# Performance work log

Hardware: AMD Instinct MI355X
Metric: run time of the kernel (lower is better)

Reference implementation:

```python
import jax, jax.numpy as jnp
import numpy as np

D_MODEL = 1024
N_HEADS = 16
D_HEAD = 64
D_MLP = 4096
EPS = 1e-5
IGNORE = -1e5
ATTN_SCALE = float(np.sqrt(D_HEAD))


def setup_inputs() -> dict:
    key = jax.random.key(0)
    ks = jax.random.split(key, 10)
    s = 0.02
    return {
        "x": jax.random.normal(ks[0], (2, 2048, D_MODEL), jnp.float32),
        "ln1_w": jnp.ones((D_MODEL,), jnp.float32),
        "ln1_b": jnp.zeros((D_MODEL,), jnp.float32),
        "W_Q": jax.random.normal(ks[1], (N_HEADS, D_MODEL, D_HEAD), jnp.float32) * s,
        "W_K": jax.random.normal(ks[2], (N_HEADS, D_MODEL, D_HEAD), jnp.float32) * s,
        "W_V": jax.random.normal(ks[3], (N_HEADS, D_MODEL, D_HEAD), jnp.float32) * s,
        "W_O": jax.random.normal(ks[4], (N_HEADS, D_HEAD, D_MODEL), jnp.float32) * s,
        "b_Q": jnp.zeros((N_HEADS, D_HEAD), jnp.float32),
        "b_K": jnp.zeros((N_HEADS, D_HEAD), jnp.float32),
        "b_V": jnp.zeros((N_HEADS, D_HEAD), jnp.float32),
        "b_O": jnp.zeros((D_MODEL,), jnp.float32),
        "ln2_w": jnp.ones((D_MODEL,), jnp.float32),
        "ln2_b": jnp.zeros((D_MODEL,), jnp.float32),
        "W_in": jax.random.normal(ks[5], (D_MODEL, D_MLP), jnp.float32) * s,
        "b_in": jnp.zeros((D_MLP,), jnp.float32),
        "W_out": jax.random.normal(ks[6], (D_MLP, D_MODEL), jnp.float32) * s,
        "b_out": jnp.zeros((D_MODEL,), jnp.float32),
    }


def layer_norm(x, w, b):
    x = x - x.mean(axis=-1, keepdims=True)
    scale = jnp.sqrt((x * x).mean(axis=-1, keepdims=True) + EPS)
    return (x / scale) * w + b


def attention(x, W_Q, W_K, W_V, W_O, b_Q, b_K, b_V, b_O):
    # x: [b, s, d_model]; W_{Q,K,V}: [h, d_model, d_head]
    q = jnp.einsum('bsm,hmd->bshd', x, W_Q) + b_Q
    k = jnp.einsum('bsm,hmd->bshd', x, W_K) + b_K
    v = jnp.einsum('bsm,hmd->bshd', x, W_V) + b_V
    scores = jnp.einsum('bqhd,bkhd->bhqk', q, k) / ATTN_SCALE
    s = x.shape[1]
    mask = jnp.tril(jnp.ones((s, s), bool))  # causal
    scores = jnp.where(mask, scores, IGNORE)
    attn = jax.nn.softmax(scores, axis=-1)
    z = jnp.einsum('bkhd,bhqk->bqhd', v, attn)
    return jnp.einsum('bqhd,hdm->bqm', z, W_O) + b_O


def mlp(x, W_in, b_in, W_out, b_out):
    pre = jnp.einsum('bsm,mf->bsf', x, W_in) + b_in
    post = jax.nn.gelu(pre, approximate=False)
    return jnp.einsum('bsf,fm->bsm', post, W_out) + b_out


def reference(x, ln1_w, ln1_b, W_Q, W_K, W_V, W_O, b_Q, b_K, b_V, b_O,
              ln2_w, ln2_b, W_in, b_in, W_out, b_out):
    resid = x + attention(layer_norm(x, ln1_w, ln1_b), W_Q, W_K, W_V, W_O,
                          b_Q, b_K, b_V, b_O)
    out = resid + mlp(layer_norm(resid, ln2_w, ln2_b), W_in, b_in, W_out, b_out)
    return out
```

## Files before the change

### kernel.cpp

```cpp
#include <hip/hip_runtime.h>

typedef __attribute__((ext_vector_type(4))) float f32x4;
typedef __attribute__((ext_vector_type(8))) __bf16 bf16x8;
typedef __attribute__((ext_vector_type(8))) unsigned short ushort8;
typedef __attribute__((ext_vector_type(4))) unsigned short ushort4v;

union UBF8 { ushort8 u; bf16x8 b; };
static __device__ __forceinline__ bf16x8 as_bf(ushort8 v) { UBF8 x; x.u = v; return x.b; }

static __device__ __forceinline__ unsigned short f2bf(float f) {
  union { __bf16 h; unsigned short u; } v; v.h = (__bf16)f; return v.u;
}

static __device__ __forceinline__ unsigned short f2bf_rn(float f) {
  union { float f; unsigned u; } v; v.f = f;
  unsigned r = v.u + 0x7fffu + ((v.u >> 16) & 1u);
  return (unsigned short)(r >> 16);
}

static __device__ __forceinline__ bf16x8 scale8(ushort8 u, float c) {
  ushort8 r;
#pragma unroll
  for (int j = 0; j < 8; j++) {
    union { unsigned u; float f; } t; t.u = ((unsigned)u[j]) << 16;
    r[j] = f2bf_rn(t.f * c);
  }
  return as_bf(r);
}

static __device__ __forceinline__ float gelu_f(float x) {
  return 0.5f * x * (1.0f + erff(x * 0.70710678118654752f));
}

typedef const __attribute__((address_space(1))) void* gas_p;
typedef __attribute__((address_space(3))) void* las_p;
static __device__ __forceinline__ void gload16(const void* g, void* l) {
  __builtin_amdgcn_global_load_lds((gas_p)g, (las_p)l, 16, 0, 0);
}

__global__ __launch_bounds__(256) void ln_kernel(
    const float* __restrict__ in, const float* __restrict__ w,
    const float* __restrict__ b, unsigned short* __restrict__ out)
{
  const int row = blockIdx.x, t = threadIdx.x;
  const float4 v = *reinterpret_cast<const float4*>(in + (size_t)row * 1024 + t * 4);
  float s = v.x + v.y + v.z + v.w;
#pragma unroll
  for (int o = 32; o >= 1; o >>= 1) s += __shfl_xor(s, o);
  __shared__ float ps[4], qs[4];
  if ((t & 63) == 0) ps[t >> 6] = s;
  __syncthreads();
  const float mean = (ps[0] + ps[1] + ps[2] + ps[3]) * (1.0f / 1024.0f);
  const float cx = v.x - mean, cy = v.y - mean, cz = v.z - mean, cw = v.w - mean;
  float q = cx * cx + cy * cy + cz * cz + cw * cw;
#pragma unroll
  for (int o = 32; o >= 1; o >>= 1) q += __shfl_xor(q, o);
  if ((t & 63) == 0) qs[t >> 6] = q;
  __syncthreads();
  const float rstd = rsqrtf((qs[0] + qs[1] + qs[2] + qs[3]) * (1.0f / 1024.0f) + 1e-5f);
  const float4 wv = *reinterpret_cast<const float4*>(w + t * 4);
  const float4 bv = *reinterpret_cast<const float4*>(b + t * 4);
  ushort4v o4;
  o4.x = f2bf(cx * rstd * wv.x + bv.x);
  o4.y = f2bf(cy * rstd * wv.y + bv.y);
  o4.z = f2bf(cz * rstd * wv.z + bv.z);
  o4.w = f2bf(cw * rstd * wv.w + bv.w);
  *reinterpret_cast<ushort4v*>(out + (size_t)row * 1024 + t * 4) = o4;
}

__global__ __launch_bounds__(256) void conv_qkv_kernel(
    const float* __restrict__ WQ, const float* __restrict__ WK,
    const float* __restrict__ WV, unsigned short* __restrict__ out)
{
  __shared__ float t[32][33];
  const int mat_h = blockIdx.z;
  const int mat = mat_h >> 4, h = mat_h & 15;
  const float* W = (mat == 0 ? WQ : (mat == 1 ? WK : WV)) + (size_t)h * (1024 * 64);
  const int m0 = blockIdx.x * 32;
  const int d0 = blockIdx.y * 32;
  const int tx = threadIdx.x & 31, ty = threadIdx.x >> 5;
#pragma unroll
  for (int j = 0; j < 4; j++)
    t[ty + j * 8][tx] = W[(size_t)(m0 + ty + j * 8) * 64 + d0 + tx];
  __syncthreads();
  const size_t obase = (size_t)(mat * 1024 + h * 64 + d0);
#pragma unroll
  for (int j = 0; j < 4; j++)
    out[(obase + ty + j * 8) * 1024 + m0 + tx] = f2bf(t[tx][ty + j * 8]);
}

__global__ __launch_bounds__(256) void pack_bias_kernel(
    const float* __restrict__ bQ, const float* __restrict__ bK,
    const float* __restrict__ bV, float* __restrict__ out)
{
  const int i = blockIdx.x * 256 + threadIdx.x;
  if (i < 1024) out[i] = bQ[i];
  else if (i < 2048) out[i] = bK[i - 1024];
  else if (i < 3072) out[i] = bV[i - 2048];
}

__global__ __launch_bounds__(256) void transpose_cast_kernel(
    const float* __restrict__ in, unsigned short* __restrict__ out, int R, int C)
{
  __shared__ float t[32][33];
  const int c0 = blockIdx.x * 32, r0 = blockIdx.y * 32;
  const int tx = threadIdx.x & 31, ty = threadIdx.x >> 5;
#pragma unroll
  for (int j = 0; j < 4; j++)
    t[ty + j * 8][tx] = in[(size_t)(r0 + ty + j * 8) * C + c0 + tx];
  __syncthreads();
#pragma unroll
  for (int j = 0; j < 4; j++)
    out[(size_t)(c0 + ty + j * 8) * R + r0 + tx] = f2bf(t[tx][ty + j * 8]);
}

template <int BN, int EPI, int WAVES>
__global__ __launch_bounds__(WAVES * 64) void gemm_kernel(
    const unsigned short* __restrict__ A, const unsigned short* __restrict__ Bt,
    void* Cout, const float* __restrict__ bias, const float* resid,
    int N, int K, int gx)
{
  constexpr int BM = 128, BK = 64;
  constexpr int NF = (BN * 2) / (WAVES * 16);
  constexpr int CA = (BM / 8) / WAVES;
  constexpr int CB = (BN / 8) / WAVES;
  __shared__ __align__(16) unsigned short As[2][BM * BK];
  __shared__ __align__(16) unsigned short Bs[2][BN * BK];
  const int tid = threadIdx.x, lane = tid & 63, w = tid >> 6;
  const int nwg = gridDim.x;
  int id = blockIdx.x;
  id = (id & 7) * (nwg >> 3) + (id >> 3);
  const int bm = (id % gx) * BM, bn = (id / gx) * BN;

  const int l15 = lane & 15, hi = lane >> 4;
  const int arow = (WAVES == 8) ? (w >> 2) * 64 : (w >> 1) * 64;
  const int brow = (WAVES == 8) ? (w & 3) * (BN / 4) : (w & 1) * (BN / 2);
  f32x4 acc[4][NF] = {};

  const int srow = lane >> 3;
  const int scol = ((lane & 7) ^ srow) * 8;
  const unsigned short* Ag[CA];
  const unsigned short* Bg[CB];
#pragma unroll
  for (int it = 0; it < CA; it++)
    Ag[it] = A + (size_t)(bm + 8 * (it * WAVES + w) + srow) * K + scol;
#pragma unroll
  for (int it = 0; it < CB; it++)
    Bg[it] = Bt + (size_t)(bn + 8 * (it * WAVES + w) + srow) * K + scol;

  const int rsw = (l15 & 7) << 4;
  const int NT = K / BK;

  auto stage = [&](int k0, int buf) {
#pragma unroll
    for (int it = 0; it < CA; it++)
      gload16(Ag[it] + k0, &As[buf][(it * WAVES + w) * 512]);
#pragma unroll
    for (int it = 0; it < CB; it++)
      gload16(Bg[it] + k0, &Bs[buf][(it * WAVES + w) * 512]);
  };

  stage(0, 0);
  __syncthreads();
  int cur = 0;

  for (int t = 0; t < NT; ++t) {
    if (t + 1 < NT) stage((t + 1) * BK, cur ^ 1);

    const char* Asb = (const char*)As[cur];
    const char* Bsb = (const char*)Bs[cur];
    bf16x8 af[2][4], bfr[2][NF];
#pragma unroll
    for (int kk = 0; kk < 2; kk++) {
      const int cb = kk * 64 + hi * 16;
#pragma unroll
      for (int mf = 0; mf < 4; mf++) {
        const int R = arow + mf * 16 + l15;
        af[kk][mf] = as_bf(*reinterpret_cast<const ushort8*>(Asb + R * (BK * 2) + (cb ^ rsw)));
      }
#pragma unroll
      for (int nf = 0; nf < NF; nf++) {
        const int R = brow + nf * 16 + l15;
        bfr[kk][nf] = as_bf(*reinterpret_cast<const ushort8*>(Bsb + R * (BK * 2) + (cb ^ rsw)));
      }
    }
#pragma unroll
    for (int kk = 0; kk < 2; kk++)
#pragma unroll
      for (int mf = 0; mf < 4; mf++)
#pragma unroll
        for (int nf = 0; nf < NF; nf++)
          acc[mf][nf] = __builtin_amdgcn_mfma_f32_16x16x32_bf16(af[kk][mf], bfr[kk][nf], acc[mf][nf], 0, 0, 0);

    __syncthreads();
    cur ^= 1;
  }

  const int row0 = bm + arow + 4 * hi;
  const int col0 = bn + brow + l15;
#pragma unroll
  for (int mf = 0; mf < 4; mf++) {
#pragma unroll
    for (int nf = 0; nf < NF; nf++) {
#pragma unroll
      for (int i = 0; i < 4; i++) {
        const int row = row0 + mf * 16 + i;
        const int col = col0 + nf * 16;
        float v = acc[mf][nf][i] + bias[col];
        if (EPI == 1) v += resid[(size_t)row * N + col];
        if (EPI == 2) v = gelu_f(v);
        if (EPI == 1) ((float*)Cout)[(size_t)row * N + col] = v;
        else          ((unsigned short*)Cout)[(size_t)row * N + col] = f2bf(v);
      }
    }
  }
}

__global__ __launch_bounds__(256) void attn_kernel(
    const unsigned short* __restrict__ qkv, unsigned short* __restrict__ zout)
{
  __shared__ __align__(16) unsigned short Ks[64 * 72];
  __shared__ __align__(16) unsigned short Vt[64 * 72];
  __shared__ __align__(16) unsigned short Ps[4 * 16 * 72];
  const int tid = threadIdx.x, lane = tid & 63, w = tid >> 6;
  const int l15 = lane & 15, hi = lane >> 4, ko = hi * 8;
  const int j = blockIdx.x, bh = blockIdx.y;
  const int cA = j, cB = 31 - j;
  const size_t tok0 = (size_t)(bh >> 4) * 2048;
  const int h = bh & 15;
  const int qoff = h * 64, koff = 1024 + h * 64, voff = 2048 + h * 64;
  const int rowA = cA * 64 + w * 16;
  const int rowB = cB * 64 + w * 16;
  const float qscale = 0.125f * 1.44269504f;

  bf16x8 qfA[2], qfB[2];
#pragma unroll
  for (int kf = 0; kf < 2; kf++) {
    qfA[kf] = scale8(*reinterpret_cast<const ushort8*>(qkv + (tok0 + rowA + l15) * 3072 + qoff + kf * 32 + ko), qscale);
    qfB[kf] = scale8(*reinterpret_cast<const ushort8*>(qkv + (tok0 + rowB + l15) * 3072 + qoff + kf * 32 + ko), qscale);
  }

  float mA[4], lA[4], mB[4], lB[4];
  f32x4 zA[4], zB[4];
#pragma unroll
  for (int i = 0; i < 4; i++) {
    mA[i] = -1e30f; lA[i] = 0.0f; mB[i] = -1e30f; lB[i] = 0.0f;
#pragma unroll
    for (int nf = 0; nf < 4; nf++) { zA[nf][i] = 0.0f; zB[nf][i] = 0.0f; }
  }

  unsigned short* Pw = Ps + w * (16 * 72);
  const int sr = tid >> 3, scol = (tid & 7) * 8;

  for (int kt = 0; kt <= cB; kt++) {
    __syncthreads();
#pragma unroll
    for (int it = 0; it < 2; it++) {
      const int rr = sr + it * 32;
      const size_t gb = (tok0 + kt * 64 + rr) * 3072;
      *reinterpret_cast<ushort8*>(&Ks[rr * 72 + scol]) =
          *reinterpret_cast<const ushort8*>(qkv + gb + koff + scol);
      ushort8 vv = *reinterpret_cast<const ushort8*>(qkv + gb + voff + scol);
#pragma unroll
      for (int jj = 0; jj < 8; jj++) {
        const int d = scol + jj;
        Vt[d * 72 + (rr ^ (((d >> 3) & 7) << 3))] = vv[jj];
      }
    }
    __syncthreads();

    bf16x8 kb[4][2], vb[4][2];
#pragma unroll
    for (int nf = 0; nf < 4; nf++)
#pragma unroll
      for (int kf = 0; kf < 2; kf++) {
        kb[nf][kf] = as_bf(*reinterpret_cast<const ushort8*>(&Ks[(nf * 16 + l15) * 72 + kf * 32 + ko]));
        const int d = nf * 16 + l15;
        vb[nf][kf] = as_bf(*reinterpret_cast<const ushort8*>(
            &Vt[d * 72 + ((kf * 32 + ko) ^ (((d >> 3) & 7) << 3))]));
      }

    const bool actA = (kt <= cA);

    f32x4 sA[4] = {}, sB[4] = {};
    __builtin_amdgcn_s_setprio(1);
#pragma unroll
    for (int nf = 0; nf < 4; nf++)
#pragma unroll
      for (int kf = 0; kf < 2; kf++) {
        if (actA) sA[nf] = __builtin_amdgcn_mfma_f32_16x16x32_bf16(qfA[kf], kb[nf][kf], sA[nf], 0, 0, 0);
        sB[nf] = __builtin_amdgcn_mfma_f32_16x16x32_bf16(qfB[kf], kb[nf][kf], sB[nf], 0, 0, 0);
      }
    __builtin_amdgcn_s_setprio(0);

    auto process = [&](f32x4* s, float* mrow, float* lrow, f32x4* accz, int rowbase, bool dm) {
#pragma unroll
      for (int i = 0; i < 4; i++) {
        const int rg = rowbase + 4 * hi + i;
        float mx = -1e30f;
#pragma unroll
        for (int nf = 0; nf < 4; nf++) {
          float v = s[nf][i];
          if (dm && (kt * 64 + nf * 16 + l15 > rg)) v = -1e30f;
          s[nf][i] = v;
          mx = fmaxf(mx, v);
        }
#pragma unroll
        for (int o = 1; o <= 8; o <<= 1) mx = fmaxf(mx, __shfl_xor(mx, o));
        const float mnew = fmaxf(mrow[i], mx);
        const float fct = exp2f(mrow[i] - mnew);
        mrow[i] = mnew;
        float rs = 0.0f;
#pragma unroll
        for (int nf = 0; nf < 4; nf++) {
          const float pv = exp2f(s[nf][i] - mnew);
          s[nf][i] = pv;
          rs += pv;
        }
#pragma unroll
        for (int o = 1; o <= 8; o <<= 1) rs += __shfl_xor(rs, o);
        lrow[i] = lrow[i] * fct + rs;
#pragma unroll
        for (int nf = 0; nf < 4; nf++) accz[nf][i] *= fct;
      }
#pragma unroll
      for (int i = 0; i < 4; i++)
#pragma unroll
        for (int nf = 0; nf < 4; nf++)
          Pw[(4 * hi + i) * 72 + ((nf * 16 + l15) ^ (hi << 3))] = f2bf_rn(s[nf][i]);
#pragma unroll
      for (int kf = 0; kf < 2; kf++) {
        const bf16x8 pa = as_bf(*reinterpret_cast<const ushort8*>(
            &Pw[l15 * 72 + ((kf * 32 + ko) ^ (((l15 >> 2) & 3) << 3))]));
        __builtin_amdgcn_s_setprio(1);
#pragma unroll
        for (int nf = 0; nf < 4; nf++)
          accz[nf] = __builtin_amdgcn_mfma_f32_16x16x32_bf16(pa, vb[nf][kf], accz[nf], 0, 0, 0);
        __builtin_amdgcn_s_setprio(0);
      }
    };

    if (actA) process(sA, mA, lA, zA, rowA, kt >= cA);
    process(sB, mB, lB, zB, rowB, kt >= cB);
  }

  auto wb = [&](float* lrow, f32x4* accz, int rowbase) {
#pragma unroll
    for (int i = 0; i < 4; i++) {
      const float inv = 1.0f / lrow[i];
      const int srow = rowbase + 4 * hi + i;
#pragma unroll
      for (int nf = 0; nf < 4; nf++)
        zout[(tok0 + srow) * 1024 + h * 64 + nf * 16 + l15] = f2bf_rn(accz[nf][i] * inv);
    }
  };
  wb(lA, zA, rowA);
  wb(lB, zB, rowB);
}

extern "C" void kernel_launch(void* const* d_in, const int* in_sizes, int n_in,
                              void* d_out, int out_size, void* d_ws, size_t ws_size,
                              hipStream_t stream)
{
  const float* x    = (const float*)d_in[0];
  const float* ln1w = (const float*)d_in[1];
  const float* ln1b = (const float*)d_in[2];
  const float* WQ   = (const float*)d_in[3];
  const float* WK   = (const float*)d_in[4];
  const float* WV   = (const float*)d_in[5];
  const float* WO   = (const float*)d_in[6];
  const float* bQ   = (const float*)d_in[7];
  const float* bK   = (const float*)d_in[8];
  const float* bV   = (const float*)d_in[9];
  const float* bO   = (const float*)d_in[10];
  const float* ln2w = (const float*)d_in[11];
  const float* ln2b = (const float*)d_in[12];
  const float* Win  = (const float*)d_in[13];
  const float* bin  = (const float*)d_in[14];
  const float* Wout = (const float*)d_in[15];
  const float* bout = (const float*)d_in[16];
  float* out = (float*)d_out;

  char* ws = (char*)d_ws;
  unsigned short* bufA   = (unsigned short*)ws;
  unsigned short* bufB   = (unsigned short*)(ws + (size_t)(32 << 20));
  unsigned short* bufC   = (unsigned short*)(ws + (size_t)(40 << 20));
  float*          biasQKV = (float*)(ws + (size_t)(48 << 20));

  ln_kernel<<<4096, 256, 0, stream>>>(x, ln1w, ln1b, bufB);
  conv_qkv_kernel<<<dim3(32, 2, 48), 256, 0, stream>>>(WQ, WK, WV, bufC);
  pack_bias_kernel<<<12, 256, 0, stream>>>(bQ, bK, bV, biasQKV);
  gemm_kernel<128, 0, 8><<<768, 512, 0, stream>>>(bufB, bufC, bufA, biasQKV, nullptr, 3072, 1024, 32);
  attn_kernel<<<dim3(16, 32), 256, 0, stream>>>(bufA, bufB);
  transpose_cast_kernel<<<dim3(32, 32), 256, 0, stream>>>(WO, bufC, 1024, 1024);
  gemm_kernel<64, 1, 8><<<512, 512, 0, stream>>>(bufB, bufC, out, bO, x, 1024, 1024, 32);
  ln_kernel<<<4096, 256, 0, stream>>>(out, ln2w, ln2b, bufB);
  transpose_cast_kernel<<<dim3(128, 32), 256, 0, stream>>>(Win, bufC, 1024, 4096);
  gemm_kernel<128, 2, 8><<<1024, 512, 0, stream>>>(bufB, bufC, bufA, bin, nullptr, 4096, 1024, 32);
  transpose_cast_kernel<<<dim3(32, 128), 256, 0, stream>>>(Wout, bufC, 4096, 1024);
  gemm_kernel<64, 1, 8><<<512, 512, 0, stream>>>(bufA, bufC, out, bout, out, 1024, 4096, 32);
}
```

Before: 292.6 us.

## Replace paired causal query tiles with one tile per block, heaviest first

The attention kernel used to give each block two query tiles (j and 31-j) so every block did balanced causal work and K/V tiles loaded into LDS were shared across both. Now each block handles a single 64-row query tile, launched in descending order of causal length, and the grid doubles to 1024 blocks. This is meant to raise parallelism and cut per-thread register pressure, which may raise occupancy. In exchange each K/V tile is loaded from global memory and staged through LDS twice as often, and blocks are no longer balanced, so the scheduler has to even out the load.

```diff
diff --git a/kernel.cpp b/kernel.cpp
--- a/kernel.cpp
+++ b/kernel.cpp
@@ -224,35 +224,32 @@
   __shared__ __align__(16) unsigned short Ps[4 * 16 * 72];
   const int tid = threadIdx.x, lane = tid & 63, w = tid >> 6;
   const int l15 = lane & 15, hi = lane >> 4, ko = hi * 8;
-  const int j = blockIdx.x, bh = blockIdx.y;
-  const int cA = j, cB = 31 - j;
+  const int c = 31 - blockIdx.x;
+  const int bh = blockIdx.y;
   const size_t tok0 = (size_t)(bh >> 4) * 2048;
   const int h = bh & 15;
   const int qoff = h * 64, koff = 1024 + h * 64, voff = 2048 + h * 64;
-  const int rowA = cA * 64 + w * 16;
-  const int rowB = cB * 64 + w * 16;
+  const int row = c * 64 + w * 16;
   const float qscale = 0.125f * 1.44269504f;
 
-  bf16x8 qfA[2], qfB[2];
-#pragma unroll
-  for (int kf = 0; kf < 2; kf++) {
-    qfA[kf] = scale8(*reinterpret_cast<const ushort8*>(qkv + (tok0 + rowA + l15) * 3072 + qoff + kf * 32 + ko), qscale);
-    qfB[kf] = scale8(*reinterpret_cast<const ushort8*>(qkv + (tok0 + rowB + l15) * 3072 + qoff + kf * 32 + ko), qscale);
-  }
-
-  float mA[4], lA[4], mB[4], lB[4];
-  f32x4 zA[4], zB[4];
+  bf16x8 qf[2];
+#pragma unroll
+  for (int kf = 0; kf < 2; kf++)
+    qf[kf] = scale8(*reinterpret_cast<const ushort8*>(qkv + (tok0 + row + l15) * 3072 + qoff + kf * 32 + ko), qscale);
+
+  float m[4], l[4];
+  f32x4 z[4];
 #pragma unroll
   for (int i = 0; i < 4; i++) {
-    mA[i] = -1e30f; lA[i] = 0.0f; mB[i] = -1e30f; lB[i] = 0.0f;
-#pragma unroll
-    for (int nf = 0; nf < 4; nf++) { zA[nf][i] = 0.0f; zB[nf][i] = 0.0f; }
+    m[i] = -1e30f; l[i] = 0.0f;
+#pragma unroll
+    for (int nf = 0; nf < 4; nf++) z[nf][i] = 0.0f;
   }
 
   unsigned short* Pw = Ps + w * (16 * 72);
   const int sr = tid >> 3, scol = (tid & 7) * 8;
 
-  for (int kt = 0; kt <= cB; kt++) {
+  for (int kt = 0; kt <= c; kt++) {
     __syncthreads();
 #pragma unroll
     for (int it = 0; it < 2; it++) {
@@ -280,82 +277,70 @@
             &Vt[d * 72 + ((kf * 32 + ko) ^ (((d >> 3) & 7) << 3))]));
       }
 
-    const bool actA = (kt <= cA);
-
-    f32x4 sA[4] = {}, sB[4] = {};
+    f32x4 s[4] = {};
     __builtin_amdgcn_s_setprio(1);
 #pragma unroll
     for (int nf = 0; nf < 4; nf++)
 #pragma unroll
-      for (int kf = 0; kf < 2; kf++) {
-        if (actA) sA[nf] = __builtin_amdgcn_mfma_f32_16x16x32_bf16(qfA[kf], kb[nf][kf], sA[nf], 0, 0, 0);
-        sB[nf] = __builtin_amdgcn_mfma_f32_16x16x32_bf16(qfB[kf], kb[nf][kf], sB[nf], 0, 0, 0);
-      }
+      for (int kf = 0; kf < 2; kf++)
+        s[nf] = __builtin_amdgcn_mfma_f32_16x16x32_bf16(qf[kf], kb[nf][kf], s[nf], 0, 0, 0);
     __builtin_amdgcn_s_setprio(0);
 
-    auto process = [&](f32x4* s, float* mrow, float* lrow, f32x4* accz, int rowbase, bool dm) {
-#pragma unroll
-      for (int i = 0; i < 4; i++) {
-        const int rg = rowbase + 4 * hi + i;
-        float mx = -1e30f;
-#pragma unroll
-        for (int nf = 0; nf < 4; nf++) {
-          float v = s[nf][i];
-          if (dm && (kt * 64 + nf * 16 + l15 > rg)) v = -1e30f;
-          s[nf][i] = v;
-          mx = fmaxf(mx, v);
-        }
-#pragma unroll
-        for (int o = 1; o <= 8; o <<= 1) mx = fmaxf(mx, __shfl_xor(mx, o));
-        const float mnew = fmaxf(mrow[i], mx);
-        const float fct = exp2f(mrow[i] - mnew);
-        mrow[i] = mnew;
-        float rs = 0.0f;
-#pragma unroll
-        for (int nf = 0; nf < 4; nf++) {
-          const float pv = exp2f(s[nf][i] - mnew);
-          s[nf][i] = pv;
-          rs += pv;
-        }
-#pragma unroll
-        for (int o = 1; o <= 8; o <<= 1) rs += __shfl_xor(rs, o);
-        lrow[i] = lrow[i] * fct + rs;
-#pragma unroll
-        for (int nf = 0; nf < 4; nf++) accz[nf][i] *= fct;
-      }
-#pragma unroll
-      for (int i = 0; i < 4; i++)
-#pragma unroll
-        for (int nf = 0; nf < 4; nf++)
-          Pw[(4 * hi + i) * 72 + ((nf * 16 + l15) ^ (hi << 3))] = f2bf_rn(s[nf][i]);
-#pragma unroll
-      for (int kf = 0; kf < 2; kf++) {
-        const bf16x8 pa = as_bf(*reinterpret_cast<const ushort8*>(
-            &Pw[l15 * 72 + ((kf * 32 + ko) ^ (((l15 >> 2) & 3) << 3))]));
-        __builtin_amdgcn_s_setprio(1);
-#pragma unroll
-        for (int nf = 0; nf < 4; nf++)
-          accz[nf] = __builtin_amdgcn_mfma_f32_16x16x32_bf16(pa, vb[nf][kf], accz[nf], 0, 0, 0);
-        __builtin_amdgcn_s_setprio(0);
-      }
-    };
-
-    if (actA) process(sA, mA, lA, zA, rowA, kt >= cA);
-    process(sB, mB, lB, zB, rowB, kt >= cB);
-  }
-
-  auto wb = [&](float* lrow, f32x4* accz, int rowbase) {
+    const bool dm = (kt == c);
 #pragma unroll
     for (int i = 0; i < 4; i++) {
-      const float inv = 1.0f / lrow[i];
-      const int srow = rowbase + 4 * hi + i;
+      const int rg = row + 4 * hi + i;
+      float mx = -1e30f;
+#pragma unroll
+      for (int nf = 0; nf < 4; nf++) {
+        float v = s[nf][i];
+        if (dm && (kt * 64 + nf * 16 + l15 > rg)) v = -1e30f;
+        s[nf][i] = v;
+        mx = fmaxf(mx, v);
+      }
+#pragma unroll
+      for (int o = 1; o <= 8; o <<= 1) mx = fmaxf(mx, __shfl_xor(mx, o));
+      const float mnew = fmaxf(m[i], mx);
+      const float fct = exp2f(m[i] - mnew);
+      m[i] = mnew;
+      float rs = 0.0f;
+#pragma unroll
+      for (int nf = 0; nf < 4; nf++) {
+        const float pv = exp2f(s[nf][i] - mnew);
+        s[nf][i] = pv;
+        rs += pv;
+      }
+#pragma unroll
+      for (int o = 1; o <= 8; o <<= 1) rs += __shfl_xor(rs, o);
+      l[i] = l[i] * fct + rs;
+#pragma unroll
+      for (int nf = 0; nf < 4; nf++) z[nf][i] *= fct;
+    }
+#pragma unroll
+    for (int i = 0; i < 4; i++)
 #pragma unroll
       for (int nf = 0; nf < 4; nf++)
-        zout[(tok0 + srow) * 1024 + h * 64 + nf * 16 + l15] = f2bf_rn(accz[nf][i] * inv);
-    }
-  };
-  wb(lA, zA, rowA);
-  wb(lB, zB, rowB);
+        Pw[(4 * hi + i) * 72 + ((nf * 16 + l15) ^ (hi << 3))] = f2bf_rn(s[nf][i]);
+#pragma unroll
+    for (int kf = 0; kf < 2; kf++) {
+      const bf16x8 pa = as_bf(*reinterpret_cast<const ushort8*>(
+          &Pw[l15 * 72 + ((kf * 32 + ko) ^ (((l15 >> 2) & 3) << 3))]));
+      __builtin_amdgcn_s_setprio(1);
+#pragma unroll
+      for (int nf = 0; nf < 4; nf++)
+        z[nf] = __builtin_amdgcn_mfma_f32_16x16x32_bf16(pa, vb[nf][kf], z[nf], 0, 0, 0);
+      __builtin_amdgcn_s_setprio(0);
+    }
+  }
+
+#pragma unroll
+  for (int i = 0; i < 4; i++) {
+    const float inv = 1.0f / l[i];
+    const int srw = row + 4 * hi + i;
+#pragma unroll
+    for (int nf = 0; nf < 4; nf++)
+      zout[(tok0 + srw) * 1024 + h * 64 + nf * 16 + l15] = f2bf_rn(z[nf][i] * inv);
+  }
 }
 
 extern "C" void kernel_launch(void* const* d_in, const int* in_sizes, int n_in,
@@ -391,7 +376,7 @@
   conv_qkv_kernel<<<dim3(32, 2, 48), 256, 0, stream>>>(WQ, WK, WV, bufC);
   pack_bias_kernel<<<12, 256, 0, stream>>>(bQ, bK, bV, biasQKV);
   gemm_kernel<128, 0, 8><<<768, 512, 0, stream>>>(bufB, bufC, bufA, biasQKV, nullptr, 3072, 1024, 32);
-  attn_kernel<<<dim3(16, 32), 256, 0, stream>>>(bufA, bufB);
+  attn_kernel<<<dim3(32, 32), 256, 0, stream>>>(bufA, bufB);
   transpose_cast_kernel<<<dim3(32, 32), 256, 0, stream>>>(WO, bufC, 1024, 1024);
   gemm_kernel<64, 1, 8><<<512, 512, 0, stream>>>(bufB, bufC, out, bO, x, 1024, 1024, 32);
   ln_kernel<<<4096, 256, 0, stream>>>(out, ln2w, ln2b, bufB);
```

Result: slower. 354.8 us (+21.2%).

## Prefetch two K-tiles ahead with explicit vmcnt waits in GEMM loop

Applied to the files above, without the earlier changes.

Reworks the GEMM main loop so two tiles are in flight. After computing on a buffer, the kernel refills that same buffer with tile t+2 and waits with s_waitcnt vmcnt only for the older loads, instead of a full __syncthreads drain. The goal is to hide global-to-LDS latency behind MFMA work. The cost is extra barriers per iteration. The waves layout is also hardcoded to 8 waves, which would break a 4-wave instantiation, and the vmcnt counts assume a fixed number of loads per stage.

```diff
diff --git a/kernel.cpp b/kernel.cpp
--- a/kernel.cpp
+++ b/kernel.cpp
@@ -124,6 +124,7 @@
   constexpr int NF = (BN * 2) / (WAVES * 16);
   constexpr int CA = (BM / 8) / WAVES;
   constexpr int CB = (BN / 8) / WAVES;
+  constexpr int L = CA + CB;
   __shared__ __align__(16) unsigned short As[2][BM * BK];
   __shared__ __align__(16) unsigned short Bs[2][BN * BK];
   const int tid = threadIdx.x, lane = tid & 63, w = tid >> 6;
@@ -133,8 +134,8 @@
   const int bm = (id % gx) * BM, bn = (id / gx) * BN;
 
   const int l15 = lane & 15, hi = lane >> 4;
-  const int arow = (WAVES == 8) ? (w >> 2) * 64 : (w >> 1) * 64;
-  const int brow = (WAVES == 8) ? (w & 3) * (BN / 4) : (w & 1) * (BN / 2);
+  const int arow = (w >> 2) * 64;
+  const int brow = (w & 3) * (BN / 4);
   f32x4 acc[4][NF] = {};
 
   const int srow = lane >> 3;
@@ -160,13 +161,20 @@
       gload16(Bg[it] + k0, &Bs[buf][(it * WAVES + w) * 512]);
   };
 
+#define WAIT_VM_L()                                                      \
+  do {                                                                   \
+    if constexpr (L == 4) asm volatile("s_waitcnt vmcnt(4)" ::: "memory"); \
+    else                  asm volatile("s_waitcnt vmcnt(3)" ::: "memory"); \
+  } while (0)
+
   stage(0, 0);
-  __syncthreads();
-  int cur = 0;
+  stage(BK, 1);
+  WAIT_VM_L();
+  __builtin_amdgcn_s_barrier();
+  asm volatile("" ::: "memory");
 
   for (int t = 0; t < NT; ++t) {
-    if (t + 1 < NT) stage((t + 1) * BK, cur ^ 1);
-
+    const int cur = t & 1;
     const char* Asb = (const char*)As[cur];
     const char* Bsb = (const char*)Bs[cur];
     bf16x8 af[2][4], bfr[2][NF];
@@ -192,9 +200,22 @@
         for (int nf = 0; nf < NF; nf++)
           acc[mf][nf] = __builtin_amdgcn_mfma_f32_16x16x32_bf16(af[kk][mf], bfr[kk][nf], acc[mf][nf], 0, 0, 0);
 
-    __syncthreads();
-    cur ^= 1;
-  }
+    asm volatile("s_waitcnt lgkmcnt(0)" ::: "memory");
+    __builtin_amdgcn_s_barrier();
+    asm volatile("" ::: "memory");
+
+    if (t + 2 < NT) {
+      stage((t + 2) * BK, cur);
+      WAIT_VM_L();
+      __builtin_amdgcn_s_barrier();
+      asm volatile("" ::: "memory");
+    } else if (t + 1 < NT) {
+      asm volatile("s_waitcnt vmcnt(0)" ::: "memory");
+      __builtin_amdgcn_s_barrier();
+      asm volatile("" ::: "memory");
+    }
+  }
+#undef WAIT_VM_L
 
   const int row0 = bm + arow + 4 * hi;
   const int col0 = bn + brow + l15;
```

Result: slower. 301.8 us (+3.1%).
